# Optimization experiments

Hardware: AMD Instinct MI355X
Metric: run time of the kernel (lower is better)

## Reference

```python
import jax, jax.numpy as jnp
import numpy as np

N = 100000   # nodes
E = 1600000  # edges (avg degree 16)
IN, H, HID, OUT = 128, 2, 64, 32


def setup_inputs() -> dict:
    key = jax.random.key(0)
    ks = jax.random.split(key, 20)
    def p(k, shape, scale=0.1):
        return jax.random.normal(k, shape, jnp.float32) * scale
    inp = {
        "x": jax.random.normal(ks[0], (N, IN), jnp.float32),
        "edge_index": jax.random.randint(ks[1], (2, E), 0, N),
    }
    # per-layer params: W [din, H*dout], att_src/att_dst [H, dout], bias
    dims = [(IN, HID), (H * HID, HID), (H * HID, HID), (H * HID, OUT)]
    for i, (din, dout) in enumerate(dims):
        inp[f"W{i}"] = p(ks[2 + 4 * i], (din, H * dout))
        inp[f"asrc{i}"] = p(ks[3 + 4 * i], (H, dout))
        inp[f"adst{i}"] = p(ks[4 + 4 * i], (H, dout))
        inp[f"b{i}"] = jnp.zeros((H * dout if i < 3 else dout,), jnp.float32)
    return inp


def gat_conv(h, src, dst, W, a_s, a_d, b, concat):
    # PyG GATConv, add_self_loops=False, negative_slope=0.2, eval mode
    heads, dout = a_s.shape
    n = h.shape[0]
    xl = (h @ W).reshape(n, heads, dout)              # [N, H, D]
    alpha_src = jnp.einsum('nhd,hd->nh', xl, a_s)     # [N, H]
    alpha_dst = jnp.einsum('nhd,hd->nh', xl, a_d)
    e = alpha_src[src] + alpha_dst[dst]               # [E, H]
    e = jax.nn.leaky_relu(e, 0.2)
    # segment softmax over edges sharing a destination node
    m = jax.ops.segment_max(e, dst, num_segments=n)
    m = jnp.where(jnp.isfinite(m), m, 0.0)            # guard isolated nodes
    ex = jnp.exp(e - m[dst])
    denom = jax.ops.segment_sum(ex, dst, num_segments=n)
    alpha = ex / (denom[dst] + 1e-16)                 # [E, H]
    msg = xl[src] * alpha[:, :, None]                 # [E, H, D]
    out = jax.ops.segment_sum(msg, dst, num_segments=n)
    out = out.reshape(n, heads * dout) if concat else out.mean(axis=1)
    return out + b


def reference(x, edge_index, W0, asrc0, adst0, b0, W1, asrc1, adst1, b1,
              W2, asrc2, adst2, b2, W3, asrc3, adst3, b3):
    src, dst = edge_index[0], edge_index[1]
    layers = [
        (W0, asrc0, adst0, b0, True),
        (W1, asrc1, adst1, b1, True),
        (W2, asrc2, adst2, b2, True),
        (W3, asrc3, adst3, b3, False),
    ]
    h = x
    for i, (W, a_s, a_d, b, concat) in enumerate(layers):
        h = gat_conv(h, src, dst, W, a_s, a_d, b, concat)
        if i != len(layers) - 1:
            h = jax.nn.relu(h)
    return jax.nn.log_softmax(h, axis=-1)
```

## Files before the change

kernel.cpp:

```cpp
#include <hip/hip_runtime.h>
#include <hip/hip_bf16.h>
#include <math.h>

#define N_NODES 100000
#define N_EDGES 1600000

constexpr int SCAN_B = 1024;

constexpr int BSHIFT = 9, BMASK = 511;
constexpr int NBUCKET = (N_NODES + 511) / 512;
constexpr int BCAP = 16384;
constexpr int CAPB = 12288;
constexpr int EPT = 16, BIN_T = 256, BIN_CHUNK = BIN_T * EPT;

__device__ __forceinline__ unsigned short f2bf(float f) {
    unsigned int u = __float_as_uint(f);
    unsigned int r = (u + 0x7fff + ((u >> 16) & 1)) >> 16;
    return (unsigned short)r;
}


__global__ __launch_bounds__(BIN_T) void bin_kernel(const int* __restrict__ src,
                                                    const int* __restrict__ dst,
                                                    int* __restrict__ bcnt,
                                                    unsigned int* __restrict__ bstore, int E) {
    __shared__ int cnt[NBUCKET];
    __shared__ int base[NBUCKET];
    int t = threadIdx.x;
    for (int i = t; i < NBUCKET; i += BIN_T) cnt[i] = 0;
    __syncthreads();
    int e0 = blockIdx.x * BIN_CHUNK;
    int ssrc[EPT], sdst[EPT];
#pragma unroll
    for (int k = 0; k < EPT; ++k) {
        int e = e0 + t + k * BIN_T;
        if (e < E) {
            ssrc[k] = src[e];
            sdst[k] = dst[e];
            atomicAdd(&cnt[sdst[k] >> BSHIFT], 1);
        } else {
            sdst[k] = -1;
        }
    }
    __syncthreads();
    for (int i = t; i < NBUCKET; i += BIN_T) {
        base[i] = atomicAdd(&bcnt[i], cnt[i]);
        cnt[i] = 0;
    }
    __syncthreads();
#pragma unroll
    for (int k = 0; k < EPT; ++k) {
        if (sdst[k] >= 0) {
            int b = sdst[k] >> BSHIFT;
            int off = base[b] + atomicAdd(&cnt[b], 1);
            if (off < BCAP)
                bstore[(size_t)b * BCAP + off] =
                    ((unsigned)ssrc[k] << BSHIFT) | (unsigned)(sdst[k] & BMASK);
        }
    }
}

__global__ __launch_bounds__(256) void deg_from_buckets(const int* __restrict__ bcnt,
                                                        const unsigned int* __restrict__ bstore,
                                                        int* __restrict__ deg, int N) {
    __shared__ int dcnt[512];
    int b = blockIdx.x, t = threadIdx.x;
    for (int i = t; i < 512; i += 256) dcnt[i] = 0;
    __syncthreads();
    int cnt = min(bcnt[b], BCAP);
    for (int i = t; i < cnt; i += 256)
        atomicAdd(&dcnt[bstore[(size_t)b * BCAP + i] & BMASK], 1);
    __syncthreads();
    int nodeBase = b << BSHIFT;
    for (int i = t; i < 512; i += 256)
        if (nodeBase + i < N) deg[nodeBase + i] = dcnt[i];
}

__global__ void scan_block_kernel(const int* __restrict__ in, int* __restrict__ out,
                                  int* __restrict__ partials, int n) {
    __shared__ int sh[SCAN_B];
    int gid = blockIdx.x * SCAN_B + threadIdx.x;
    int v = (gid < n) ? in[gid] : 0;
    sh[threadIdx.x] = v;
    __syncthreads();
    for (int off = 1; off < SCAN_B; off <<= 1) {
        int x = (threadIdx.x >= (unsigned)off) ? sh[threadIdx.x - off] : 0;
        __syncthreads();
        sh[threadIdx.x] += x;
        __syncthreads();
    }
    if (gid < n) out[gid] = sh[threadIdx.x];
    if (threadIdx.x == SCAN_B - 1) partials[blockIdx.x] = sh[SCAN_B - 1];
}

__global__ void scan_partials_kernel(int* partials, int nb) {
    __shared__ int sh[SCAN_B];
    int v = (threadIdx.x < (unsigned)nb) ? partials[threadIdx.x] : 0;
    sh[threadIdx.x] = v;
    __syncthreads();
    for (int off = 1; off < SCAN_B; off <<= 1) {
        int x = (threadIdx.x >= (unsigned)off) ? sh[threadIdx.x - off] : 0;
        __syncthreads();
        sh[threadIdx.x] += x;
        __syncthreads();
    }
    if (threadIdx.x < (unsigned)nb) partials[threadIdx.x] = sh[threadIdx.x] - v;
}

__global__ void scan_add_kernel(int* out, const int* __restrict__ partials, int n) {
    int gid = blockIdx.x * SCAN_B + threadIdx.x;
    if (gid < n) out[gid] += partials[blockIdx.x];
}

__global__ __launch_bounds__(256) void build_col_kernel(const int* __restrict__ rp,
                                                        const int* __restrict__ bcnt,
                                                        const unsigned int* __restrict__ bstore,
                                                        int* __restrict__ col, int N) {
    __shared__ int colStage[CAPB];
    __shared__ int rpL[513];
    __shared__ int fillL[512];
    int b = blockIdx.x, t = threadIdx.x;
    int nodeBase = b << BSHIFT;
    int nNodes = min(512, N - nodeBase);
    for (int i = t; i <= nNodes; i += 256) rpL[i] = rp[nodeBase + i];
    for (int i = t; i < nNodes; i += 256) fillL[i] = 0;
    __syncthreads();
    int segBase = rpL[0];
    int segLen = rpL[nNodes] - segBase;
    int cnt = min(bcnt[b], BCAP);
    for (int i = t; i < cnt; i += 256) {
        unsigned e = bstore[(size_t)b * BCAP + i];
        int dl = e & BMASK;
        int sv = (int)(e >> BSHIFT);
        int pos = (rpL[dl] - segBase) + atomicAdd(&fillL[dl], 1);
        if (pos < CAPB) colStage[pos] = sv;
        else col[segBase + pos] = sv;
    }
    __syncthreads();
    int lim = min(segLen, CAPB);
    for (int i = t; i < lim; i += 256) col[segBase + i] = colStage[i];
}


template<int HD, int NPB>
__global__ void gemm_alpha_v2(const float* __restrict__ h, const float* __restrict__ W,
                              const float* __restrict__ a_s, const float* __restrict__ a_d,
                              __hip_bfloat16* __restrict__ xl, float* __restrict__ asrc,
                              float* __restrict__ adst) {
    constexpr int DIN = 128, C4 = DIN / 4;
    constexpr int G = HD / 4;
    constexpr int NSPLIT = 64 / G;
    constexpr int NPT = NPB / NSPLIT;
    constexpr int HG = G / 2;

    int node0 = blockIdx.x * NPB;
    int t = threadIdx.x;
    int cg = t % G, ns = t / G;

    __shared__ float4 hrow[NPB][C4];
    const float4* h4 = (const float4*)h;
    for (int idx = t; idx < NPB * C4; idx += 64) {
        int nn = idx / C4, kk = idx % C4;
        hrow[nn][kk] = h4[(size_t)(node0 + nn) * C4 + kk];
    }
    __syncthreads();

    const float4* W4 = (const float4*)W;
    float4 acc[NPT];
#pragma unroll
    for (int i = 0; i < NPT; ++i) acc[i] = make_float4(0.f, 0.f, 0.f, 0.f);

    for (int kc = 0; kc < C4; ++kc) {
        float4 w0 = W4[(size_t)(4 * kc + 0) * G + cg];
        float4 w1 = W4[(size_t)(4 * kc + 1) * G + cg];
        float4 w2 = W4[(size_t)(4 * kc + 2) * G + cg];
        float4 w3 = W4[(size_t)(4 * kc + 3) * G + cg];
#pragma unroll
        for (int nn = 0; nn < NPT; ++nn) {
            float4 hv = hrow[ns * NPT + nn][kc];
            acc[nn].x = fmaf(hv.w, w3.x, fmaf(hv.z, w2.x, fmaf(hv.y, w1.x, fmaf(hv.x, w0.x, acc[nn].x))));
            acc[nn].y = fmaf(hv.w, w3.y, fmaf(hv.z, w2.y, fmaf(hv.y, w1.y, fmaf(hv.x, w0.y, acc[nn].y))));
            acc[nn].z = fmaf(hv.w, w3.z, fmaf(hv.z, w2.z, fmaf(hv.y, w1.z, fmaf(hv.x, w0.z, acc[nn].z))));
            acc[nn].w = fmaf(hv.w, w3.w, fmaf(hv.z, w2.w, fmaf(hv.y, w1.w, fmaf(hv.x, w0.w, acc[nn].w))));
        }
    }

    float4 asv = ((const float4*)a_s)[cg];
    float4 adv = ((const float4*)a_d)[cg];
#pragma unroll
    for (int nn = 0; nn < NPT; ++nn) {
        int node = node0 + ns * NPT + nn;
        float4 a = acc[nn];
        uint2 u;
        u.x = (unsigned)f2bf(a.x) | ((unsigned)f2bf(a.y) << 16);
        u.y = (unsigned)f2bf(a.z) | ((unsigned)f2bf(a.w) << 16);
        ((uint2*)xl)[(size_t)node * G + cg] = u;
        float ps = a.x * asv.x + a.y * asv.y + a.z * asv.z + a.w * asv.w;
        float pd = a.x * adv.x + a.y * adv.y + a.z * adv.z + a.w * adv.w;
#pragma unroll
        for (int off = G / 4; off >= 1; off >>= 1) {
            ps += __shfl_xor(ps, off, 64);
            pd += __shfl_xor(pd, off, 64);
        }
        if ((cg & (HG - 1)) == 0) {
            int head = cg / HG;
            asrc[node * 2 + head] = ps;
            adst[node * 2 + head] = pd;
        }
    }
}


__global__ void aggregate_relu_v4(const __hip_bfloat162* __restrict__ xl2,
                                  const float2* __restrict__ a_src, const float2* __restrict__ a_dst,
                                  const int* __restrict__ rp, const int* __restrict__ col,
                                  const float* __restrict__ bias, float* __restrict__ out) {
    int node = blockIdx.x;
    int t = threadIdx.x;
    int head = t >> 5;
    int beg = rp[node], deg = rp[node + 1] - beg;
    float2 adn = a_dst[node];

    __shared__ int   snS[64];
    __shared__ float pS[2][64];

    float s0 = 0.f, s1 = 0.f;
    float ax0 = 0.f, ay0 = 0.f, ax1 = 0.f, ay1 = 0.f;
    float ax2 = 0.f, ay2 = 0.f, ax3 = 0.f, ay3 = 0.f;

    if (deg <= 64) {
        float e0 = -INFINITY, e1 = -INFINITY;
        if (t < deg) {
            int sn = col[beg + t];
            snS[t] = sn;
            float2 a = a_src[sn];
            e0 = a.x + adn.x; e0 = (e0 >= 0.f) ? e0 : 0.2f * e0;
            e1 = a.y + adn.y; e1 = (e1 >= 0.f) ? e1 : 0.2f * e1;
        }
        float m0 = e0, m1 = e1;
#pragma unroll
        for (int off = 32; off >= 1; off >>= 1) {
            m0 = fmaxf(m0, __shfl_xor(m0, off, 64));
            m1 = fmaxf(m1, __shfl_xor(m1, off, 64));
        }
        if (t < deg) {
            float p0 = __expf(e0 - m0), p1 = __expf(e1 - m1);
            pS[0][t] = p0; pS[1][t] = p1;
            s0 = p0; s1 = p1;
        }
        __syncthreads();
        int j = 0;
        for (; j + 8 <= deg; j += 8) {
            int sa = snS[j+0], sb = snS[j+1], sc = snS[j+2], sd = snS[j+3];
            int se = snS[j+4], sf = snS[j+5], sg = snS[j+6], sh = snS[j+7];
            float pa = pS[head][j+0], pb = pS[head][j+1], pc = pS[head][j+2], pd = pS[head][j+3];
            float pe = pS[head][j+4], pf = pS[head][j+5], pg = pS[head][j+6], ph = pS[head][j+7];
            __hip_bfloat162 va = xl2[(size_t)sa * 64 + t];
            __hip_bfloat162 vb = xl2[(size_t)sb * 64 + t];
            __hip_bfloat162 vc = xl2[(size_t)sc * 64 + t];
            __hip_bfloat162 vd = xl2[(size_t)sd * 64 + t];
            __hip_bfloat162 ve = xl2[(size_t)se * 64 + t];
            __hip_bfloat162 vf = xl2[(size_t)sf * 64 + t];
            __hip_bfloat162 vg = xl2[(size_t)sg * 64 + t];
            __hip_bfloat162 vh = xl2[(size_t)sh * 64 + t];
            ax0 = fmaf(pa, __bfloat162float(va.x), ax0); ay0 = fmaf(pa, __bfloat162float(va.y), ay0);
            ax1 = fmaf(pb, __bfloat162float(vb.x), ax1); ay1 = fmaf(pb, __bfloat162float(vb.y), ay1);
            ax2 = fmaf(pc, __bfloat162float(vc.x), ax2); ay2 = fmaf(pc, __bfloat162float(vc.y), ay2);
            ax3 = fmaf(pd, __bfloat162float(vd.x), ax3); ay3 = fmaf(pd, __bfloat162float(vd.y), ay3);
            ax0 = fmaf(pe, __bfloat162float(ve.x), ax0); ay0 = fmaf(pe, __bfloat162float(ve.y), ay0);
            ax1 = fmaf(pf, __bfloat162float(vf.x), ax1); ay1 = fmaf(pf, __bfloat162float(vf.y), ay1);
            ax2 = fmaf(pg, __bfloat162float(vg.x), ax2); ay2 = fmaf(pg, __bfloat162float(vg.y), ay2);
            ax3 = fmaf(ph, __bfloat162float(vh.x), ax3); ay3 = fmaf(ph, __bfloat162float(vh.y), ay3);
        }
        for (; j < deg; ++j) {
            int sn = snS[j];
            float p = pS[head][j];
            __hip_bfloat162 v = xl2[(size_t)sn * 64 + t];
            ax0 = fmaf(p, __bfloat162float(v.x), ax0);
            ay0 = fmaf(p, __bfloat162float(v.y), ay0);
        }
    } else {
        float m0 = -INFINITY, m1 = -INFINITY;
        for (int j = t; j < deg; j += 64) {
            float2 a = a_src[col[beg + j]];
            float e0 = a.x + adn.x; e0 = (e0 >= 0.f) ? e0 : 0.2f * e0;
            float e1 = a.y + adn.y; e1 = (e1 >= 0.f) ? e1 : 0.2f * e1;
            m0 = fmaxf(m0, e0); m1 = fmaxf(m1, e1);
        }
#pragma unroll
        for (int off = 32; off >= 1; off >>= 1) {
            m0 = fmaxf(m0, __shfl_xor(m0, off, 64));
            m1 = fmaxf(m1, __shfl_xor(m1, off, 64));
        }
        for (int c0 = 0; c0 < deg; c0 += 64) {
            int csz = min(64, deg - c0);
            if (t < csz) {
                int sn = col[beg + c0 + t];
                float2 a = a_src[sn];
                float e0 = a.x + adn.x; e0 = (e0 >= 0.f) ? e0 : 0.2f * e0;
                float e1 = a.y + adn.y; e1 = (e1 >= 0.f) ? e1 : 0.2f * e1;
                float p0 = __expf(e0 - m0), p1 = __expf(e1 - m1);
                snS[t] = sn; pS[0][t] = p0; pS[1][t] = p1;
                s0 += p0; s1 += p1;
            }
            __syncthreads();
            for (int j = 0; j < csz; ++j) {
                int sn = snS[j];
                float p = pS[head][j];
                __hip_bfloat162 v = xl2[(size_t)sn * 64 + t];
                ax0 = fmaf(p, __bfloat162float(v.x), ax0);
                ay0 = fmaf(p, __bfloat162float(v.y), ay0);
            }
            __syncthreads();
        }
    }
#pragma unroll
    for (int off = 32; off >= 1; off >>= 1) {
        s0 += __shfl_xor(s0, off, 64);
        s1 += __shfl_xor(s1, off, 64);
    }
    float s = head ? s1 : s0;
    float inv = 1.0f / (s + 1e-16f);
    float2 b2 = ((const float2*)bias)[t];
    float ox = fmaxf(fmaf(ax0 + ax1 + ax2 + ax3, inv, b2.x), 0.f);
    float oy = fmaxf(fmaf(ay0 + ay1 + ay2 + ay3, inv, b2.y), 0.f);
    ((float2*)out)[(size_t)node * 64 + t] = make_float2(ox, oy);
}

__global__ void aggregate_final_v4(const __hip_bfloat16* __restrict__ xl,
                                   const float2* __restrict__ a_src, const float2* __restrict__ a_dst,
                                   const int* __restrict__ rp, const int* __restrict__ col,
                                   const float* __restrict__ bias, float* __restrict__ out) {
    int node = blockIdx.x;
    int t = threadIdx.x;
    int head = t >> 5;
    int beg = rp[node], deg = rp[node + 1] - beg;
    float2 adn = a_dst[node];

    __shared__ int   snS[64];
    __shared__ float pS[2][64];

    float s0 = 0.f, s1 = 0.f;
    float a0 = 0.f, a1 = 0.f, a2 = 0.f, a3 = 0.f;

    if (deg <= 64) {
        float e0 = -INFINITY, e1 = -INFINITY;
        if (t < deg) {
            int sn = col[beg + t];
            snS[t] = sn;
            float2 a = a_src[sn];
            e0 = a.x + adn.x; e0 = (e0 >= 0.f) ? e0 : 0.2f * e0;
            e1 = a.y + adn.y; e1 = (e1 >= 0.f) ? e1 : 0.2f * e1;
        }
        float m0 = e0, m1 = e1;
#pragma unroll
        for (int off = 32; off >= 1; off >>= 1) {
            m0 = fmaxf(m0, __shfl_xor(m0, off, 64));
            m1 = fmaxf(m1, __shfl_xor(m1, off, 64));
        }
        if (t < deg) {
            float p0 = __expf(e0 - m0), p1 = __expf(e1 - m1);
            pS[0][t] = p0; pS[1][t] = p1;
            s0 = p0; s1 = p1;
        }
        __syncthreads();
        int j = 0;
        for (; j + 8 <= deg; j += 8) {
            int sa = snS[j+0], sb = snS[j+1], sc = snS[j+2], sd = snS[j+3];
            int se = snS[j+4], sf = snS[j+5], sg = snS[j+6], sh = snS[j+7];
            float pa = pS[head][j+0], pb = pS[head][j+1], pc = pS[head][j+2], pd = pS[head][j+3];
            float pe = pS[head][j+4], pf = pS[head][j+5], pg = pS[head][j+6], ph = pS[head][j+7];
            float va = __bfloat162float(xl[(size_t)sa * 64 + t]);
            float vb = __bfloat162float(xl[(size_t)sb * 64 + t]);
            float vc = __bfloat162float(xl[(size_t)sc * 64 + t]);
            float vd = __bfloat162float(xl[(size_t)sd * 64 + t]);
            float ve = __bfloat162float(xl[(size_t)se * 64 + t]);
            float vf = __bfloat162float(xl[(size_t)sf * 64 + t]);
            float vg = __bfloat162float(xl[(size_t)sg * 64 + t]);
            float vh = __bfloat162float(xl[(size_t)sh * 64 + t]);
            a0 = fmaf(pa, va, a0); a1 = fmaf(pb, vb, a1);
            a2 = fmaf(pc, vc, a2); a3 = fmaf(pd, vd, a3);
            a0 = fmaf(pe, ve, a0); a1 = fmaf(pf, vf, a1);
            a2 = fmaf(pg, vg, a2); a3 = fmaf(ph, vh, a3);
        }
        for (; j < deg; ++j) {
            a0 = fmaf(pS[head][j], __bfloat162float(xl[(size_t)snS[j] * 64 + t]), a0);
        }
    } else {
        float m0 = -INFINITY, m1 = -INFINITY;
        for (int j = t; j < deg; j += 64) {
            float2 a = a_src[col[beg + j]];
            float e0 = a.x + adn.x; e0 = (e0 >= 0.f) ? e0 : 0.2f * e0;
            float e1 = a.y + adn.y; e1 = (e1 >= 0.f) ? e1 : 0.2f * e1;
            m0 = fmaxf(m0, e0); m1 = fmaxf(m1, e1);
        }
#pragma unroll
        for (int off = 32; off >= 1; off >>= 1) {
            m0 = fmaxf(m0, __shfl_xor(m0, off, 64));
            m1 = fmaxf(m1, __shfl_xor(m1, off, 64));
        }
        for (int c0 = 0; c0 < deg; c0 += 64) {
            int csz = min(64, deg - c0);
            if (t < csz) {
                int sn = col[beg + c0 + t];
                float2 a = a_src[sn];
                float e0 = a.x + adn.x; e0 = (e0 >= 0.f) ? e0 : 0.2f * e0;
                float e1 = a.y + adn.y; e1 = (e1 >= 0.f) ? e1 : 0.2f * e1;
                float p0 = __expf(e0 - m0), p1 = __expf(e1 - m1);
                snS[t] = sn; pS[0][t] = p0; pS[1][t] = p1;
                s0 += p0; s1 += p1;
            }
            __syncthreads();
            for (int j = 0; j < csz; ++j) {
                a0 = fmaf(pS[head][j], __bfloat162float(xl[(size_t)snS[j] * 64 + t]), a0);
            }
            __syncthreads();
        }
    }
#pragma unroll
    for (int off = 32; off >= 1; off >>= 1) {
        s0 += __shfl_xor(s0, off, 64);
        s1 += __shfl_xor(s1, off, 64);
    }
    float s = head ? s1 : s0;
    float o = (a0 + a1 + a2 + a3) / (s + 1e-16f);
    float other = __shfl_down(o, 32, 64);
    if (t < 32) {
        float v = 0.5f * (o + other) + bias[t];
        float mx = v;
#pragma unroll
        for (int off = 16; off >= 1; off >>= 1) mx = fmaxf(mx, __shfl_xor(mx, off, 32));
        float ex = __expf(v - mx);
        float sm = ex;
#pragma unroll
        for (int off = 16; off >= 1; off >>= 1) sm += __shfl_xor(sm, off, 32);
        out[(size_t)node * 32 + t] = v - mx - logf(sm);
    }
}


extern "C" void kernel_launch(void* const* d_in, const int* in_sizes, int n_in,
                              void* d_out, int out_size, void* d_ws, size_t ws_size,
                              hipStream_t stream) {
    const int N = N_NODES, E = N_EDGES;

    const float* x  = (const float*)d_in[0];
    const int*  ei  = (const int*)d_in[1];
    const float* W0 = (const float*)d_in[2];
    const float* as0 = (const float*)d_in[3];
    const float* ad0 = (const float*)d_in[4];
    const float* b0 = (const float*)d_in[5];
    const float* W1 = (const float*)d_in[6];
    const float* as1 = (const float*)d_in[7];
    const float* ad1 = (const float*)d_in[8];
    const float* b1 = (const float*)d_in[9];
    const float* W2 = (const float*)d_in[10];
    const float* as2 = (const float*)d_in[11];
    const float* ad2 = (const float*)d_in[12];
    const float* b2 = (const float*)d_in[13];
    const float* W3 = (const float*)d_in[14];
    const float* as3 = (const float*)d_in[15];
    const float* ad3 = (const float*)d_in[16];
    const float* b3 = (const float*)d_in[17];
    float* out = (float*)d_out;

    const int* srcv = ei;
    const int* dstv = ei + E;

    char* p = (char*)d_ws;
    auto carve = [&](size_t bytes) -> void* {
        void* r = (void*)p;
        p += (bytes + 255) & ~(size_t)255;
        return r;
    };
    int* deg      = (int*)carve((size_t)N * 4);
    int* rp       = (int*)carve((size_t)(N + 1) * 4);
    int* col      = (int*)carve((size_t)E * 4);
    int* partials = (int*)carve((size_t)SCAN_B * 4);
    int* bcnt     = (int*)carve((size_t)NBUCKET * 4);
    unsigned int* bstore = (unsigned int*)carve((size_t)NBUCKET * BCAP * 4);
    __hip_bfloat16* bufX = (__hip_bfloat16*)carve((size_t)N * 128 * 2);
    float* bufH   = (float*)carve((size_t)N * 128 * 4);
    float* asrc   = (float*)carve((size_t)N * 2 * 4);
    float* adst   = (float*)carve((size_t)N * 2 * 4);

    hipMemsetAsync(bcnt, 0, (size_t)NBUCKET * 4, stream);
    hipMemsetAsync(rp, 0, 4, stream);

    bin_kernel<<<(E + BIN_CHUNK - 1) / BIN_CHUNK, BIN_T, 0, stream>>>(srcv, dstv, bcnt, bstore, E);
    deg_from_buckets<<<NBUCKET, 256, 0, stream>>>(bcnt, bstore, deg, N);
    int nb = (N + SCAN_B - 1) / SCAN_B;
    scan_block_kernel<<<nb, SCAN_B, 0, stream>>>(deg, rp + 1, partials, N);
    scan_partials_kernel<<<1, SCAN_B, 0, stream>>>(partials, nb);
    scan_add_kernel<<<nb, SCAN_B, 0, stream>>>(rp + 1, partials, N);
    build_col_kernel<<<NBUCKET, 256, 0, stream>>>(rp, bcnt, bstore, col, N);

    constexpr int NPB = 16;
    const __hip_bfloat162* bufX2 = (const __hip_bfloat162*)bufX;
    const float2* asrc2 = (const float2*)asrc;
    const float2* adst2 = (const float2*)adst;

    gemm_alpha_v2<128, NPB><<<N / NPB, 64, 0, stream>>>(x, W0, as0, ad0, bufX, asrc, adst);
    aggregate_relu_v4<<<N, 64, 0, stream>>>(bufX2, asrc2, adst2, rp, col, b0, bufH);
    gemm_alpha_v2<128, NPB><<<N / NPB, 64, 0, stream>>>(bufH, W1, as1, ad1, bufX, asrc, adst);
    aggregate_relu_v4<<<N, 64, 0, stream>>>(bufX2, asrc2, adst2, rp, col, b1, bufH);
    gemm_alpha_v2<128, NPB><<<N / NPB, 64, 0, stream>>>(bufH, W2, as2, ad2, bufX, asrc, adst);
    aggregate_relu_v4<<<N, 64, 0, stream>>>(bufX2, asrc2, adst2, rp, col, b2, bufH);
    gemm_alpha_v2<64, NPB><<<N / NPB, 64, 0, stream>>>(bufH, W3, as3, ad3, bufX, asrc, adst);
    aggregate_final_v4<<<N, 64, 0, stream>>>(bufX, asrc2, adst2, rp, col, b3, out);
}
```

Baseline: 644.2 us.

## Replace scalar FP32 node GEMM with bf16 MFMA and pre-transposed bf16 weights

Each layer's per-node projection is rewritten to use 16x16x32 bf16 MFMA instructions instead of scalar FP32 FMAs. Input rows are converted to bf16 in shared memory, and weights are transposed and packed to bf16 by a small kernel launched up front. Attention logits are reduced from the MFMA accumulators with lane shuffles, and outputs are staged through shared memory for coalesced bf16 stores. This trades FP32 input and weight precision for matrix-core throughput and adds four small transpose launches.

```diff
diff --git a/kernel.cpp b/kernel.cpp
--- a/kernel.cpp
+++ b/kernel.cpp
@@ -12,6 +12,9 @@
 constexpr int BCAP = 16384;
 constexpr int CAPB = 12288;
 constexpr int EPT = 16, BIN_T = 256, BIN_CHUNK = BIN_T * EPT;
+
+typedef __attribute__((ext_vector_type(8))) short bf16x8;
+typedef __attribute__((ext_vector_type(4))) float f32x4;
 
 __device__ __forceinline__ unsigned short f2bf(float f) {
     unsigned int u = __float_as_uint(f);
@@ -141,72 +144,115 @@
     for (int i = t; i < lim; i += 256) col[segBase + i] = colStage[i];
 }
 
-
-template<int HD, int NPB>
-__global__ void gemm_alpha_v2(const float* __restrict__ h, const float* __restrict__ W,
-                              const float* __restrict__ a_s, const float* __restrict__ a_d,
-                              __hip_bfloat16* __restrict__ xl, float* __restrict__ asrc,
-                              float* __restrict__ adst) {
-    constexpr int DIN = 128, C4 = DIN / 4;
-    constexpr int G = HD / 4;
-    constexpr int NSPLIT = 64 / G;
-    constexpr int NPT = NPB / NSPLIT;
-    constexpr int HG = G / 2;
-
-    int node0 = blockIdx.x * NPB;
+__global__ void transpose_w_kernel(const float* __restrict__ W, unsigned int* __restrict__ Wt, int C) {
+    int idx = blockIdx.x * blockDim.x + threadIdx.x;
+    if (idx >= C * 64) return;
+    int c = idx >> 6, kk = idx & 63;
+    float w0 = W[(2 * kk) * C + c];
+    float w1 = W[(2 * kk + 1) * C + c];
+    Wt[c * 64 + kk] = (unsigned)f2bf(w0) | ((unsigned)f2bf(w1) << 16);
+}
+
+
+template<int HD>
+__global__ __launch_bounds__(64) void gemm_alpha_mfma(
+    const float* __restrict__ h, const unsigned short* __restrict__ Wt,
+    const float* __restrict__ a_s, const float* __restrict__ a_d,
+    __hip_bfloat16* __restrict__ xl, float* __restrict__ asrc, float* __restrict__ adst) {
+    constexpr int NT = HD / 16;
+    constexpr int GR = HD / 4;
+    int node0 = blockIdx.x * 16;
     int t = threadIdx.x;
-    int cg = t % G, ns = t / G;
-
-    __shared__ float4 hrow[NPB][C4];
+    int lan = t & 15, grp = t >> 4;
+
+    __shared__ unsigned short hb[16][136];
+    __shared__ float ob[16][HD + 4];
+
     const float4* h4 = (const float4*)h;
-    for (int idx = t; idx < NPB * C4; idx += 64) {
-        int nn = idx / C4, kk = idx % C4;
-        hrow[nn][kk] = h4[(size_t)(node0 + nn) * C4 + kk];
-    }
-    __syncthreads();
-
-    const float4* W4 = (const float4*)W;
-    float4 acc[NPT];
-#pragma unroll
-    for (int i = 0; i < NPT; ++i) acc[i] = make_float4(0.f, 0.f, 0.f, 0.f);
-
-    for (int kc = 0; kc < C4; ++kc) {
-        float4 w0 = W4[(size_t)(4 * kc + 0) * G + cg];
-        float4 w1 = W4[(size_t)(4 * kc + 1) * G + cg];
-        float4 w2 = W4[(size_t)(4 * kc + 2) * G + cg];
-        float4 w3 = W4[(size_t)(4 * kc + 3) * G + cg];
-#pragma unroll
-        for (int nn = 0; nn < NPT; ++nn) {
-            float4 hv = hrow[ns * NPT + nn][kc];
-            acc[nn].x = fmaf(hv.w, w3.x, fmaf(hv.z, w2.x, fmaf(hv.y, w1.x, fmaf(hv.x, w0.x, acc[nn].x))));
-            acc[nn].y = fmaf(hv.w, w3.y, fmaf(hv.z, w2.y, fmaf(hv.y, w1.y, fmaf(hv.x, w0.y, acc[nn].y))));
-            acc[nn].z = fmaf(hv.w, w3.z, fmaf(hv.z, w2.z, fmaf(hv.y, w1.z, fmaf(hv.x, w0.z, acc[nn].z))));
-            acc[nn].w = fmaf(hv.w, w3.w, fmaf(hv.z, w2.w, fmaf(hv.y, w1.w, fmaf(hv.x, w0.w, acc[nn].w))));
-        }
-    }
-
-    float4 asv = ((const float4*)a_s)[cg];
-    float4 adv = ((const float4*)a_d)[cg];
-#pragma unroll
-    for (int nn = 0; nn < NPT; ++nn) {
-        int node = node0 + ns * NPT + nn;
-        float4 a = acc[nn];
+#pragma unroll
+    for (int it = 0; it < 8; ++it) {
+        int idx = it * 64 + t;
+        int nn = idx >> 5, kk = idx & 31;
+        float4 v = h4[(size_t)(node0 + nn) * 32 + kk];
+        ushort4 u;
+        u.x = f2bf(v.x); u.y = f2bf(v.y); u.z = f2bf(v.z); u.w = f2bf(v.w);
+        *(ushort4*)&hb[nn][kk * 4] = u;
+    }
+    __syncthreads();
+
+    bf16x8 af[4];
+#pragma unroll
+    for (int ks = 0; ks < 4; ++ks)
+        af[ks] = *(const bf16x8*)&hb[lan][ks * 32 + grp * 8];
+
+    f32x4 acc[NT];
+#pragma unroll
+    for (int i = 0; i < NT; ++i) acc[i] = (f32x4){0.f, 0.f, 0.f, 0.f};
+
+#pragma unroll
+    for (int ks = 0; ks < 4; ++ks) {
+        bf16x8 bf[NT];
+#pragma unroll
+        for (int nt = 0; nt < NT; ++nt)
+            bf[nt] = *(const bf16x8*)(Wt + (size_t)(nt * 16 + lan) * 128 + ks * 32 + grp * 8);
+#pragma unroll
+        for (int nt = 0; nt < NT; ++nt)
+            acc[nt] = __builtin_amdgcn_mfma_f32_16x16x32_bf16(af[ks], bf[nt], acc[nt], 0, 0, 0);
+    }
+
+    float av[NT], dv[NT];
+#pragma unroll
+    for (int nt = 0; nt < NT; ++nt) {
+        av[nt] = a_s[nt * 16 + lan];
+        dv[nt] = a_d[nt * 16 + lan];
+    }
+    float psum[2][4] = {{0.f,0.f,0.f,0.f},{0.f,0.f,0.f,0.f}};
+    float pdum[2][4] = {{0.f,0.f,0.f,0.f},{0.f,0.f,0.f,0.f}};
+#pragma unroll
+    for (int nt = 0; nt < NT; ++nt) {
+        int hs = (nt >= NT / 2) ? 1 : 0;
+#pragma unroll
+        for (int j = 0; j < 4; ++j) {
+            psum[hs][j] = fmaf(acc[nt][j], av[nt], psum[hs][j]);
+            pdum[hs][j] = fmaf(acc[nt][j], dv[nt], pdum[hs][j]);
+        }
+    }
+#pragma unroll
+    for (int off = 1; off <= 8; off <<= 1) {
+#pragma unroll
+        for (int hs = 0; hs < 2; ++hs)
+#pragma unroll
+            for (int j = 0; j < 4; ++j) {
+                psum[hs][j] += __shfl_xor(psum[hs][j], off, 64);
+                pdum[hs][j] += __shfl_xor(pdum[hs][j], off, 64);
+            }
+    }
+    if (lan == 0) {
+#pragma unroll
+        for (int j = 0; j < 4; ++j) {
+            int node = node0 + grp * 4 + j;
+            asrc[node * 2 + 0] = psum[0][j];
+            asrc[node * 2 + 1] = psum[1][j];
+            adst[node * 2 + 0] = pdum[0][j];
+            adst[node * 2 + 1] = pdum[1][j];
+        }
+    }
+
+#pragma unroll
+    for (int nt = 0; nt < NT; ++nt)
+#pragma unroll
+        for (int j = 0; j < 4; ++j)
+            ob[grp * 4 + j][nt * 16 + lan] = acc[nt][j];
+    __syncthreads();
+#pragma unroll
+    for (int it = 0; it < 16 * GR / 64; ++it) {
+        int idx = it * 64 + t;
+        int nn = idx / GR, g = idx % GR;
+        float4 v = *(const float4*)&ob[nn][g * 4];
         uint2 u;
-        u.x = (unsigned)f2bf(a.x) | ((unsigned)f2bf(a.y) << 16);
-        u.y = (unsigned)f2bf(a.z) | ((unsigned)f2bf(a.w) << 16);
-        ((uint2*)xl)[(size_t)node * G + cg] = u;
-        float ps = a.x * asv.x + a.y * asv.y + a.z * asv.z + a.w * asv.w;
-        float pd = a.x * adv.x + a.y * adv.y + a.z * adv.z + a.w * adv.w;
-#pragma unroll
-        for (int off = G / 4; off >= 1; off >>= 1) {
-            ps += __shfl_xor(ps, off, 64);
-            pd += __shfl_xor(pd, off, 64);
-        }
-        if ((cg & (HG - 1)) == 0) {
-            int head = cg / HG;
-            asrc[node * 2 + head] = ps;
-            adst[node * 2 + head] = pd;
-        }
+        u.x = (unsigned)f2bf(v.x) | ((unsigned)f2bf(v.y) << 16);
+        u.y = (unsigned)f2bf(v.z) | ((unsigned)f2bf(v.w) << 16);
+        ((uint2*)xl)[(size_t)(node0 + nn) * GR + g] = u;
     }
 }
 
@@ -483,9 +529,18 @@
     float* bufH   = (float*)carve((size_t)N * 128 * 4);
     float* asrc   = (float*)carve((size_t)N * 2 * 4);
     float* adst   = (float*)carve((size_t)N * 2 * 4);
+    unsigned short* Wt0 = (unsigned short*)carve((size_t)128 * 128 * 2);
+    unsigned short* Wt1 = (unsigned short*)carve((size_t)128 * 128 * 2);
+    unsigned short* Wt2 = (unsigned short*)carve((size_t)128 * 128 * 2);
+    unsigned short* Wt3 = (unsigned short*)carve((size_t)64 * 128 * 2);
 
     hipMemsetAsync(bcnt, 0, (size_t)NBUCKET * 4, stream);
     hipMemsetAsync(rp, 0, 4, stream);
+
+    transpose_w_kernel<<<(128 * 64 + 255) / 256, 256, 0, stream>>>(W0, (unsigned int*)Wt0, 128);
+    transpose_w_kernel<<<(128 * 64 + 255) / 256, 256, 0, stream>>>(W1, (unsigned int*)Wt1, 128);
+    transpose_w_kernel<<<(128 * 64 + 255) / 256, 256, 0, stream>>>(W2, (unsigned int*)Wt2, 128);
+    transpose_w_kernel<<<(64 * 64 + 255) / 256, 256, 0, stream>>>(W3, (unsigned int*)Wt3, 64);
 
     bin_kernel<<<(E + BIN_CHUNK - 1) / BIN_CHUNK, BIN_T, 0, stream>>>(srcv, dstv, bcnt, bstore, E);
     deg_from_buckets<<<NBUCKET, 256, 0, stream>>>(bcnt, bstore, deg, N);
@@ -495,17 +550,16 @@
     scan_add_kernel<<<nb, SCAN_B, 0, stream>>>(rp + 1, partials, N);
     build_col_kernel<<<NBUCKET, 256, 0, stream>>>(rp, bcnt, bstore, col, N);
 
-    constexpr int NPB = 16;
     const __hip_bfloat162* bufX2 = (const __hip_bfloat162*)bufX;
     const float2* asrc2 = (const float2*)asrc;
     const float2* adst2 = (const float2*)adst;
 
-    gemm_alpha_v2<128, NPB><<<N / NPB, 64, 0, stream>>>(x, W0, as0, ad0, bufX, asrc, adst);
+    gemm_alpha_mfma<128><<<N / 16, 64, 0, stream>>>(x, Wt0, as0, ad0, bufX, asrc, adst);
     aggregate_relu_v4<<<N, 64, 0, stream>>>(bufX2, asrc2, adst2, rp, col, b0, bufH);
-    gemm_alpha_v2<128, NPB><<<N / NPB, 64, 0, stream>>>(bufH, W1, as1, ad1, bufX, asrc, adst);
+    gemm_alpha_mfma<128><<<N / 16, 64, 0, stream>>>(bufH, Wt1, as1, ad1, bufX, asrc, adst);
     aggregate_relu_v4<<<N, 64, 0, stream>>>(bufX2, asrc2, adst2, rp, col, b1, bufH);
-    gemm_alpha_v2<128, NPB><<<N / NPB, 64, 0, stream>>>(bufH, W2, as2, ad2, bufX, asrc, adst);
+    gemm_alpha_mfma<128><<<N / 16, 64, 0, stream>>>(bufH, Wt2, as2, ad2, bufX, asrc, adst);
     aggregate_relu_v4<<<N, 64, 0, stream>>>(bufX2, asrc2, adst2, rp, col, b2, bufH);
-    gemm_alpha_v2<64, NPB><<<N / NPB, 64, 0, stream>>>(bufH, W3, as3, ad3, bufX, asrc, adst);
+    gemm_alpha_mfma<64><<<N / 16, 64, 0, stream>>>(bufH, Wt3, as3, ad3, bufX, asrc, adst);
     aggregate_final_v4<<<N, 64, 0, stream>>>(bufX, asrc2, adst2, rp, col, b3, out);
 }
```

Result: faster. 562.1 us (-12.7%).
